# Kernel optimization log

Hardware: AMD Instinct MI355X
Metric: run time of the kernel (lower is better)

The kernel has to match this reference:

```python
import jax, jax.numpy as jnp
import numpy as np

INPUT_SIZE = 512
HIDDEN_SIZE = 1024
BATCH = 64
SEQ_LEN = 512


def _xavier(key, shape):
    fan_out, fan_in = shape
    limit = float(np.sqrt(6.0 / (fan_in + fan_out)))
    return jax.random.uniform(key, shape, jnp.float32, -limit, limit)


def setup_inputs() -> dict:
    key = jax.random.key(0)
    k = jax.random.split(key, 5)
    x = jax.random.normal(k[0], (BATCH, SEQ_LEN, INPUT_SIZE), jnp.float32)
    h0 = jnp.zeros((2, BATCH, HIDDEN_SIZE), jnp.float32)
    # layer 0: input_size -> hidden_size; layer 1: hidden_size -> hidden_size
    Wxh0 = _xavier(k[1], (HIDDEN_SIZE, INPUT_SIZE))
    Whh0 = _xavier(k[2], (HIDDEN_SIZE, HIDDEN_SIZE))
    b0 = jnp.zeros((HIDDEN_SIZE,), jnp.float32)
    Wxh1 = _xavier(k[3], (HIDDEN_SIZE, HIDDEN_SIZE))
    Whh1 = _xavier(k[4], (HIDDEN_SIZE, HIDDEN_SIZE))
    b1 = jnp.zeros((HIDDEN_SIZE,), jnp.float32)
    return {"x": x, "h0": h0, "Wxh0": Wxh0, "Whh0": Whh0, "b0": b0,
            "Wxh1": Wxh1, "Whh1": Whh1, "b1": b1}


def _rnn_layer(x_seq, h_init, Wxh, Whh, b):
    # Precompute the input projection for all timesteps (one big GEMM).
    # x_seq: [B, T, I] -> xproj: [B, T, H]
    xproj = jnp.einsum('bti,hi->bth', x_seq, Wxh) + b
    xproj_t = jnp.swapaxes(xproj, 0, 1)  # [T, B, H] for scan

    def step(h_prev, xp_t):
        h_t = jnp.tanh(xp_t + h_prev @ Whh.T)
        return h_t, h_t

    h_last, outs = jax.lax.scan(step, h_init, xproj_t)
    return jnp.swapaxes(outs, 0, 1), h_last  # [B, T, H], [B, H]


def reference(x, h0, Wxh0, Whh0, b0, Wxh1, Whh1, b1):
    out0, hn0 = _rnn_layer(x, h0[0], Wxh0, Whh0, b0)
    out1, hn1 = _rnn_layer(out0, h0[1], Wxh1, Whh1, b1)
    h_n = jnp.stack([hn0, hn1], axis=0)  # [num_layers, B, H]
    return out1, h_n
```

## Files before the change

### kernel.cpp

```cpp
#include <hip/hip_runtime.h>
#include <hip/hip_fp16.h>

typedef _Float16 f16;
typedef unsigned int u32;
typedef unsigned short u16;
typedef unsigned long long u64;
typedef _Float16 f16x8 __attribute__((ext_vector_type(8)));
typedef float f32x4 __attribute__((ext_vector_type(4)));

#define B_ 64
#define T_ 512
#define I_ 512
#define H_ 1024
#define HB_ (B_ * H_)
#define NWG_ 192
#define RS_ 32768
#define XS_ 65536

__device__ __forceinline__ u64 lda64(const u32* p) {
    return __hip_atomic_load((const u64*)p, __ATOMIC_RELAXED, __HIP_MEMORY_SCOPE_AGENT);
}
__device__ __forceinline__ u32 lda32(const u32* p) {
    return __hip_atomic_load(p, __ATOMIC_RELAXED, __HIP_MEMORY_SCOPE_AGENT);
}
__device__ __forceinline__ void sta32(u32* p, u32 v) {
    __hip_atomic_store(p, v, __ATOMIC_RELAXED, __HIP_MEMORY_SCOPE_AGENT);
}
__device__ __forceinline__ void sta16(u16* p, u16 v) {
    __hip_atomic_store(p, v, __ATOMIC_RELAXED, __HIP_MEMORY_SCOPE_AGENT);
}
__device__ __forceinline__ void stflag(int* p, int v) {
    __hip_atomic_store(p, v, __ATOMIC_RELAXED, __HIP_MEMORY_SCOPE_AGENT);
}

__device__ __forceinline__ void fastpoll(const int* p, int thr) {
    int f0, f1, f2, f3; int g = 0;
    asm volatile(
        "global_load_dword %[a], %[q], off sc0 sc1\n\t"
        "global_load_dword %[b], %[q], off sc0 sc1\n\t"
        "global_load_dword %[c], %[q], off sc0 sc1\n\t"
        "global_load_dword %[d], %[q], off sc0 sc1\n\t"
        "1:\n\t"
        "s_add_u32 %[g], %[g], 1\n\t"
        "s_cmp_gt_u32 %[g], 0x400000\n\t"
        "s_cbranch_scc1 2f\n\t"
        "s_waitcnt vmcnt(3)\n\t"
        "v_cmp_lt_i32 vcc, %[a], %[t]\n\t"
        "global_load_dword %[a], %[q], off sc0 sc1\n\t"
        "s_cbranch_vccz 2f\n\t"
        "s_waitcnt vmcnt(3)\n\t"
        "v_cmp_lt_i32 vcc, %[b], %[t]\n\t"
        "global_load_dword %[b], %[q], off sc0 sc1\n\t"
        "s_cbranch_vccz 2f\n\t"
        "s_waitcnt vmcnt(3)\n\t"
        "v_cmp_lt_i32 vcc, %[c], %[t]\n\t"
        "global_load_dword %[c], %[q], off sc0 sc1\n\t"
        "s_cbranch_vccz 2f\n\t"
        "s_waitcnt vmcnt(3)\n\t"
        "v_cmp_lt_i32 vcc, %[d], %[t]\n\t"
        "global_load_dword %[d], %[q], off sc0 sc1\n\t"
        "s_cbranch_vccnz 1b\n\t"
        "2:\n\t"
        "s_waitcnt vmcnt(0)\n\t"
        : [a]"=&v"(f0), [b]"=&v"(f1), [c]"=&v"(f2), [d]"=&v"(f3), [g]"+s"(g)
        : [q]"v"(p), [t]"v"(thr)
        : "vcc", "memory");
}

__global__ void cvt_f16(const float* __restrict__ s, f16* __restrict__ d, long n) {
    long i = ((long)blockIdx.x * blockDim.x + threadIdx.x) * 4;
    long stride = (long)gridDim.x * blockDim.x * 4;
    for (; i < n; i += stride) {
        float4 v = *reinterpret_cast<const float4*>(s + i);
        d[i+0] = (f16)v.x; d[i+1] = (f16)v.y; d[i+2] = (f16)v.z; d[i+3] = (f16)v.w;
    }
}

__global__ void init_rings(const float* __restrict__ h0,
                           u16* __restrict__ ring0, u16* __restrict__ ring1) {
    int i = blockIdx.x * blockDim.x + threadIdx.x;
    int b = i >> 10, n = i & 1023;
    int mi = b >> 4, rl = b & 15;
    int kwin = n >> 8, krem = n & 255;
    int it = krem >> 5, k32 = krem & 31;
    int kq3 = k32 >> 3, k8 = k32 & 7;
    int idx = (((mi*4 + kwin)*8 + it)*256 + (k8>>2)*128 + kq3*32 + rl*2 + ((k8>>1)&1))*2 + (k8&1);
    ring0[3*RS_*2 + idx] = __builtin_bit_cast(u16, (f16)h0[i]);
    ring1[3*RS_*2 + idx] = __builtin_bit_cast(u16, (f16)h0[HB_ + i]);
}

__global__ __launch_bounds__(256) void gemm_xproj(
    const float* __restrict__ A, const f16* __restrict__ W,
    const float* __restrict__ bias, f16* __restrict__ out)
{
    const int wave = threadIdx.x >> 6, lane = threadIdx.x & 63;
    const int m0 = blockIdx.x << 4;
    const int r = lane & 15, kq = lane >> 4;
    const int ngrp = (blockIdx.y << 9) + (wave << 7);
    const float* pa = A + (long)(m0 + r) * I_ + kq * 8;
    const f16*   pw = W + (long)(ngrp + r) * I_ + kq * 8;

    f32x4 acc[8] = {};
    #pragma unroll
    for (int kc = 0; kc < I_; kc += 32) {
        float4 a0 = *reinterpret_cast<const float4*>(pa + kc);
        float4 a1 = *reinterpret_cast<const float4*>(pa + kc + 4);
        f16x8 af = { (f16)a0.x, (f16)a0.y, (f16)a0.z, (f16)a0.w,
                     (f16)a1.x, (f16)a1.y, (f16)a1.z, (f16)a1.w };
        #pragma unroll
        for (int t = 0; t < 8; ++t) {
            f16x8 wf = *reinterpret_cast<const f16x8*>(pw + (long)t * 16 * I_ + kc);
            acc[t] = __builtin_amdgcn_mfma_f32_16x16x32_f16(af, wf, acc[t], 0, 0, 0);
        }
    }
    const int col = lane & 15, rq = lane >> 4;
    #pragma unroll
    for (int t = 0; t < 8; ++t) {
        const int n = ngrp + t * 16 + col;
        const float bv = bias[n];
        #pragma unroll
        for (int j = 0; j < 4; ++j)
            out[(long)(m0 + rq * 4 + j) * H_ + n] = (f16)(acc[t][j] + bv);
    }
}

__global__ void __launch_bounds__(256, 1) rnn_scan(
    const f16* __restrict__ Whh0, const f16* __restrict__ Wxh1, const f16* __restrict__ Whh1,
    const f16* __restrict__ xp0, const float* __restrict__ b1,
    u32* __restrict__ ring0, u32* __restrict__ ring1, u32* __restrict__ xp1,
    float* __restrict__ out, int* __restrict__ flags)
{
    extern __shared__ char smem[];
    float* part = (float*)(smem + 131072);

    const int tid = threadIdx.x;
    const int wave = tid >> 6, lane = tid & 63;
    const int wg = blockIdx.x;
    const int grp = wg >> 6, sub = wg & 63;
    const int mi = sub & 3, ct = sub >> 2;
    const int m0 = mi << 4;
    const int nbase = ct << 6;
    const int r = lane & 15, kq = lane >> 4;

    int* fAw = flags;
    int* fEw = flags + 8192;
    int* fCw = flags + 16384;
    int* fB  = flags + 24576;
    int* fD  = flags + 26624;
    const int mb4 = mi * 16;

    const f16* Wmat = (grp == 0) ? Whh0 : (grp == 1) ? Wxh1 : Whh1;

    for (int i = 0; i < 32; ++i) {
        int idx = tid + (i << 8);
        int row = idx >> 7, c = idx & 127;
        f32x4 v = *reinterpret_cast<const f32x4*>(Wmat + (long)(nbase + row) * H_ + (c << 3));
        *reinterpret_cast<f32x4*>(smem + row * 2048 + ((c ^ (row & 7)) << 4)) = v;
    }
    __syncthreads();

    const int nf = nbase + (wave << 4) + r;
    const float b1v = (grp == 1) ? b1[nf] : 0.f;

    const int kwin_s = nf >> 8, krem_s = nf & 255;
    const int it_s = krem_s >> 5, k32_s = krem_s & 31;
    const int kq3_s = k32_s >> 3, k8_s = k32_s & 7;
    const int base16 = (((mi*4 + kwin_s)*8 + it_s)*256 + (k8_s>>2)*128 + kq3_s*32 + ((k8_s>>1)&1))*2 + (k8_s&1);

    const int cBase = (mi * 4 + wave) * 2048 + (lane << 1);

    const int idx16 = lane & 15;
    const int ctp = (wave << 2) + (idx16 >> 2);
    const int wvp = idx16 & 3;
    const int myflag = ((mb4 + ct) * 4 + wave) * 32;
    const int* poll_p; int poll_d;
    if (grp == 0) {
        if (lane < 16)      { poll_p = fAw + ((mb4 + ctp) * 4 + wvp) * 32; poll_d = 0; }
        else if (lane < 32) { poll_p = fB + (mb4 + idx16) * 32;            poll_d = -3; }
        else                { poll_p = fAw + myflag;                        poll_d = -1000000; }
    } else if (grp == 1) {
        if (lane < 16)      { poll_p = fAw + ((mb4 + ctp) * 4 + wvp) * 32; poll_d = 1; }
        else if (lane == 16){ poll_p = fD + (mb4 + ct) * 32;               poll_d = -3; }
        else                { poll_p = fCw + myflag;                        poll_d = -1000000; }
    } else {
        if (lane < 16)      { poll_p = fEw + ((mb4 + ctp) * 4 + wvp) * 32; poll_d = 0; }
        else if (lane == 16){ poll_p = fCw + ((mb4 + ct) * 4 + wave) * 32; poll_d = 1; }
        else                { poll_p = fEw + myflag;                        poll_d = -1000000; }
    }

    for (int ts = 0; ts < T_; ++ts) {
        float xv[4];
        if (grp == 0) {
            #pragma unroll
            for (int j = 0; j < 4; ++j)
                xv[j] = (float)xp0[((long)(m0 + kq * 4 + j) * T_ + ts) * H_ + nf];
        } else {
            #pragma unroll
            for (int j = 0; j < 4; ++j) xv[j] = 0.f;
        }

        fastpoll(poll_p, ts + poll_d);
        __builtin_amdgcn_sched_barrier(0);

        const u32* ringA;
        if (grp == 0)      ringA = ring0 + ((ts - 1) & 3) * RS_;
        else if (grp == 1) ringA = ring0 + (ts & 3) * RS_;
        else               ringA = ring1 + ((ts - 1) & 3) * RS_;

        if (grp == 2) {
            #pragma unroll
            for (int j = 0; j < 4; ++j)
                xv[j] = __builtin_bit_cast(float,
                    lda32(xp1 + (ts & 3) * XS_ + (m0 + kq * 4 + j) * 1024 + nf));
        }

        const u32* abase = ringA + cBase;
        u64 q[8][2];
        #pragma unroll
        for (int it = 0; it < 8; ++it) {
            q[it][0] = lda64(abase + it * 256);
            q[it][1] = lda64(abase + it * 256 + 128);
        }

        f16x8 ah[8];
        #pragma unroll
        for (int it = 0; it < 8; ++it) {
            u32 w0 = (u32)q[it][0], w1 = (u32)(q[it][0] >> 32);
            u32 w2 = (u32)q[it][1], w3 = (u32)(q[it][1] >> 32);
            ah[it][0] = __builtin_bit_cast(f16, (u16)(w0 & 0xffff));
            ah[it][1] = __builtin_bit_cast(f16, (u16)(w0 >> 16));
            ah[it][2] = __builtin_bit_cast(f16, (u16)(w1 & 0xffff));
            ah[it][3] = __builtin_bit_cast(f16, (u16)(w1 >> 16));
            ah[it][4] = __builtin_bit_cast(f16, (u16)(w2 & 0xffff));
            ah[it][5] = __builtin_bit_cast(f16, (u16)(w2 >> 16));
            ah[it][6] = __builtin_bit_cast(f16, (u16)(w3 & 0xffff));
            ah[it][7] = __builtin_bit_cast(f16, (u16)(w3 >> 16));
        }
        asm volatile("s_waitcnt vmcnt(0)" ::: "memory");
        __builtin_amdgcn_sched_barrier(0);

        f32x4 acc[4] = {};
        #pragma unroll
        for (int it = 0; it < 8; ++it) {
            #pragma unroll
            for (int t = 0; t < 4; ++t) {
                f16x8 wf = *reinterpret_cast<const f16x8*>(
                    smem + (t * 16 + r) * 2048
                         + ((((wave << 5) + (it << 2) + kq) ^ (r & 7)) << 4));
                acc[t] = __builtin_amdgcn_mfma_f32_16x16x32_f16(ah[it], wf, acc[t], 0, 0, 0);
            }
        }
        #pragma unroll
        for (int t = 0; t < 4; ++t)
            *reinterpret_cast<f32x4*>(&part[((wave << 2) + t) * 256 + (lane << 2)]) = acc[t];
        __syncthreads();

        if (tid == 0) {
            if (grp == 1)      stflag(fB + (mb4 + ct) * 32, ts + 1);
            else if (grp == 2) stflag(fD + (mb4 + ct) * 32, ts + 1);
        }

        {
            f32x4 sm = *reinterpret_cast<f32x4*>(&part[wave * 256 + (lane << 2)]);
            #pragma unroll
            for (int w2 = 1; w2 < 4; ++w2)
                sm = sm + *reinterpret_cast<f32x4*>(&part[((w2 << 2) + wave) * 256 + (lane << 2)]);
            #pragma unroll
            for (int j = 0; j < 4; ++j) {
                const int b = m0 + kq * 4 + j;
                float v = sm[j];
                if (grp == 0) {
                    v = tanhf(v + xv[j]);
                    sta16((u16*)ring0 + (ts & 3) * RS_ * 2 + base16 + (kq * 4 + j) * 4,
                          __builtin_bit_cast(u16, (f16)v));
                    if (ts == T_ - 1) out[(long)B_ * T_ * H_ + (long)b * H_ + nf] = v;
                } else if (grp == 1) {
                    sta32(xp1 + (ts & 3) * XS_ + b * 1024 + nf, __builtin_bit_cast(u32, v + b1v));
                } else {
                    v = tanhf(v + xv[j]);
                    sta16((u16*)ring1 + (ts & 3) * RS_ * 2 + base16 + (kq * 4 + j) * 4,
                          __builtin_bit_cast(u16, (f16)v));
                    out[((long)b * T_ + ts) * H_ + nf] = v;
                    if (ts == T_ - 1) out[(long)B_ * T_ * H_ + HB_ + (long)b * H_ + nf] = v;
                }
            }
        }
        asm volatile("s_waitcnt vmcnt(0)" ::: "memory");
        if (lane == 0) {
            if (grp == 0)      stflag(fAw + myflag, ts + 1);
            else if (grp == 1) stflag(fCw + myflag, ts + 1);
            else               stflag(fEw + myflag, ts + 1);
        }
        __syncthreads();
    }
}

extern "C" void kernel_launch(void* const* d_in, const int* in_sizes, int n_in,
                              void* d_out, int out_size, void* d_ws, size_t ws_size,
                              hipStream_t stream) {
    const float* x    = (const float*)d_in[0];
    const float* h0   = (const float*)d_in[1];
    const float* Wxh0 = (const float*)d_in[2];
    const float* Whh0 = (const float*)d_in[3];
    const float* b0   = (const float*)d_in[4];
    const float* Wxh1 = (const float*)d_in[5];
    const float* Whh1 = (const float*)d_in[6];
    const float* b1   = (const float*)d_in[7];
    float* out = (float*)d_out;

    char* ws = (char*)d_ws;
    const long MB = 1024 * 1024;
    f16* Whh0h = (f16*)(ws + 0);
    f16* Wxh1h = (f16*)(ws + 2*MB);
    f16* Whh1h = (f16*)(ws + 4*MB);
    f16* Wxh0h = (f16*)(ws + 6*MB);
    int* flags = (int*)(ws + 7*MB);
    u32* ring0 = (u32*)(ws + 8*MB);
    u32* ring1 = (u32*)(ws + 9*MB);
    u32* xp1   = (u32*)(ws + 10*MB);
    f16* xp0   = (f16*)(ws + 16*MB);

    cvt_f16<<<512, 256, 0, stream>>>(Whh0, Whh0h, (long)H_*H_);
    cvt_f16<<<512, 256, 0, stream>>>(Wxh1, Wxh1h, (long)H_*H_);
    cvt_f16<<<512, 256, 0, stream>>>(Whh1, Whh1h, (long)H_*H_);
    cvt_f16<<<512, 256, 0, stream>>>(Wxh0, Wxh0h, (long)H_*I_);
    init_rings<<<HB_/256, 256, 0, stream>>>(h0, (u16*)ring0, (u16*)ring1);
    hipMemsetAsync(flags, 0, 128*1024, stream);

    gemm_xproj<<<dim3((B_*T_)/16, H_/512), 256, 0, stream>>>(x, Wxh0h, b0, xp0);

    hipFuncSetAttribute((const void*)rnn_scan,
                        hipFuncAttributeMaxDynamicSharedMemorySize, 147456);

    void* args[] = { (void*)&Whh0h, (void*)&Wxh1h, (void*)&Whh1h, (void*)&xp0,
                     (void*)&b1, (void*)&ring0, (void*)&ring1, (void*)&xp1,
                     (void*)&out, (void*)&flags };
    hipLaunchCooperativeKernel((void*)rnn_scan, dim3(NWG_), dim3(256), args,
                               147456, stream);
}
```

Before: 2.294 ms.

## Replace per-step flag polling with sentinel-tagged ring data and coarse progress flags

Removes the per-wave flag handshake between producer and consumer workgroups. Consumers now spin on the ring data itself until no 0xFFFF sentinel remains, and producers poison a slot a few steps ahead. The ring grows to 32 slots, and a coarse back-pressure flag is checked every 8 steps. The separate Whh/Wxh1 fp16 conversion kernels are dropped by converting fp32 weights into LDS inside the scan kernel. Risks: a real fp16 value with bit pattern 0xFFFF (a NaN) would be misread as unwritten, bounded spin loops may silently continue on timeout, and extra sentinel stores add memory traffic.

```diff
diff --git a/kernel.cpp b/kernel.cpp
--- a/kernel.cpp
+++ b/kernel.cpp
@@ -16,6 +16,8 @@
 #define NWG_ 192
 #define RS_ 32768
 #define XS_ 65536
+#define NS_ 31
+#define RL_ 8
 
 __device__ __forceinline__ u64 lda64(const u32* p) {
     return __hip_atomic_load((const u64*)p, __ATOMIC_RELAXED, __HIP_MEMORY_SCOPE_AGENT);
@@ -32,39 +34,16 @@
 __device__ __forceinline__ void stflag(int* p, int v) {
     __hip_atomic_store(p, v, __ATOMIC_RELAXED, __HIP_MEMORY_SCOPE_AGENT);
 }
-
-__device__ __forceinline__ void fastpoll(const int* p, int thr) {
-    int f0, f1, f2, f3; int g = 0;
-    asm volatile(
-        "global_load_dword %[a], %[q], off sc0 sc1\n\t"
-        "global_load_dword %[b], %[q], off sc0 sc1\n\t"
-        "global_load_dword %[c], %[q], off sc0 sc1\n\t"
-        "global_load_dword %[d], %[q], off sc0 sc1\n\t"
-        "1:\n\t"
-        "s_add_u32 %[g], %[g], 1\n\t"
-        "s_cmp_gt_u32 %[g], 0x400000\n\t"
-        "s_cbranch_scc1 2f\n\t"
-        "s_waitcnt vmcnt(3)\n\t"
-        "v_cmp_lt_i32 vcc, %[a], %[t]\n\t"
-        "global_load_dword %[a], %[q], off sc0 sc1\n\t"
-        "s_cbranch_vccz 2f\n\t"
-        "s_waitcnt vmcnt(3)\n\t"
-        "v_cmp_lt_i32 vcc, %[b], %[t]\n\t"
-        "global_load_dword %[b], %[q], off sc0 sc1\n\t"
-        "s_cbranch_vccz 2f\n\t"
-        "s_waitcnt vmcnt(3)\n\t"
-        "v_cmp_lt_i32 vcc, %[c], %[t]\n\t"
-        "global_load_dword %[c], %[q], off sc0 sc1\n\t"
-        "s_cbranch_vccz 2f\n\t"
-        "s_waitcnt vmcnt(3)\n\t"
-        "v_cmp_lt_i32 vcc, %[d], %[t]\n\t"
-        "global_load_dword %[d], %[q], off sc0 sc1\n\t"
-        "s_cbranch_vccnz 1b\n\t"
-        "2:\n\t"
-        "s_waitcnt vmcnt(0)\n\t"
-        : [a]"=&v"(f0), [b]"=&v"(f1), [c]"=&v"(f2), [d]"=&v"(f3), [g]"+s"(g)
-        : [q]"v"(p), [t]"v"(thr)
-        : "vcc", "memory");
+__device__ __forceinline__ int ldflag(const int* p) {
+    return __hip_atomic_load(p, __ATOMIC_RELAXED, __HIP_MEMORY_SCOPE_AGENT);
+}
+__device__ __forceinline__ u32 badq(u64 v) {
+    u32 lo = (u32)v, hi = (u32)(v >> 32);
+    u32 b = ((lo & 0xFFFFu) == 0xFFFFu) ? 1u : 0u;
+    b |= ((lo >> 16) == 0xFFFFu) ? 1u : 0u;
+    b |= ((hi & 0xFFFFu) == 0xFFFFu) ? 1u : 0u;
+    b |= ((hi >> 16) == 0xFFFFu) ? 1u : 0u;
+    return b;
 }
 
 __global__ void cvt_f16(const float* __restrict__ s, f16* __restrict__ d, long n) {
@@ -85,8 +64,8 @@
     int it = krem >> 5, k32 = krem & 31;
     int kq3 = k32 >> 3, k8 = k32 & 7;
     int idx = (((mi*4 + kwin)*8 + it)*256 + (k8>>2)*128 + kq3*32 + rl*2 + ((k8>>1)&1))*2 + (k8&1);
-    ring0[3*RS_*2 + idx] = __builtin_bit_cast(u16, (f16)h0[i]);
-    ring1[3*RS_*2 + idx] = __builtin_bit_cast(u16, (f16)h0[HB_ + i]);
+    ring0[NS_*RS_*2 + idx] = __builtin_bit_cast(u16, (f16)h0[i]);
+    ring1[NS_*RS_*2 + idx] = __builtin_bit_cast(u16, (f16)h0[HB_ + i]);
 }
 
 __global__ __launch_bounds__(256) void gemm_xproj(
@@ -125,7 +104,7 @@
 }
 
 __global__ void __launch_bounds__(256, 1) rnn_scan(
-    const f16* __restrict__ Whh0, const f16* __restrict__ Wxh1, const f16* __restrict__ Whh1,
+    const float* __restrict__ Whh0, const float* __restrict__ Wxh1, const float* __restrict__ Whh1,
     const f16* __restrict__ xp0, const float* __restrict__ b1,
     u32* __restrict__ ring0, u32* __restrict__ ring1, u32* __restrict__ xp1,
     float* __restrict__ out, int* __restrict__ flags)
@@ -142,20 +121,21 @@
     const int nbase = ct << 6;
     const int r = lane & 15, kq = lane >> 4;
 
-    int* fAw = flags;
-    int* fEw = flags + 8192;
-    int* fCw = flags + 16384;
-    int* fB  = flags + 24576;
-    int* fD  = flags + 26624;
+    int* prog1 = flags;
+    int* prog2 = flags + 2048;
     const int mb4 = mi * 16;
 
-    const f16* Wmat = (grp == 0) ? Whh0 : (grp == 1) ? Wxh1 : Whh1;
+    const float* Wmat = (grp == 0) ? Whh0 : (grp == 1) ? Wxh1 : Whh1;
 
     for (int i = 0; i < 32; ++i) {
         int idx = tid + (i << 8);
         int row = idx >> 7, c = idx & 127;
-        f32x4 v = *reinterpret_cast<const f32x4*>(Wmat + (long)(nbase + row) * H_ + (c << 3));
-        *reinterpret_cast<f32x4*>(smem + row * 2048 + ((c ^ (row & 7)) << 4)) = v;
+        const float* src = Wmat + (long)(nbase + row) * H_ + (c << 3);
+        float4 w0 = *reinterpret_cast<const float4*>(src);
+        float4 w1 = *reinterpret_cast<const float4*>(src + 4);
+        f16x8 wf = { (f16)w0.x, (f16)w0.y, (f16)w0.z, (f16)w0.w,
+                     (f16)w1.x, (f16)w1.y, (f16)w1.z, (f16)w1.w };
+        *reinterpret_cast<f16x8*>(smem + row * 2048 + ((c ^ (row & 7)) << 4)) = wf;
     }
     __syncthreads();
 
@@ -169,26 +149,14 @@
 
     const int cBase = (mi * 4 + wave) * 2048 + (lane << 1);
 
-    const int idx16 = lane & 15;
-    const int ctp = (wave << 2) + (idx16 >> 2);
-    const int wvp = idx16 & 3;
-    const int myflag = ((mb4 + ct) * 4 + wave) * 32;
-    const int* poll_p; int poll_d;
-    if (grp == 0) {
-        if (lane < 16)      { poll_p = fAw + ((mb4 + ctp) * 4 + wvp) * 32; poll_d = 0; }
-        else if (lane < 32) { poll_p = fB + (mb4 + idx16) * 32;            poll_d = -3; }
-        else                { poll_p = fAw + myflag;                        poll_d = -1000000; }
-    } else if (grp == 1) {
-        if (lane < 16)      { poll_p = fAw + ((mb4 + ctp) * 4 + wvp) * 32; poll_d = 1; }
-        else if (lane == 16){ poll_p = fD + (mb4 + ct) * 32;               poll_d = -3; }
-        else                { poll_p = fCw + myflag;                        poll_d = -1000000; }
-    } else {
-        if (lane < 16)      { poll_p = fEw + ((mb4 + ctp) * 4 + wvp) * 32; poll_d = 0; }
-        else if (lane == 16){ poll_p = fCw + ((mb4 + ct) * 4 + wave) * 32; poll_d = 1; }
-        else                { poll_p = fEw + myflag;                        poll_d = -1000000; }
-    }
-
     for (int ts = 0; ts < T_; ++ts) {
+        if ((ts & 7) == 0 && grp != 2 && lane < 16) {
+            const int* pf = ((grp == 0) ? prog1 : prog2) + (mb4 + lane) * 32;
+            const int thr = ts - 16;
+            int g = 0;
+            while (ldflag(pf) < thr && ++g < (1 << 20)) {}
+        }
+
         float xv[4];
         if (grp == 0) {
             #pragma unroll
@@ -199,27 +167,45 @@
             for (int j = 0; j < 4; ++j) xv[j] = 0.f;
         }
 
-        fastpoll(poll_p, ts + poll_d);
-        __builtin_amdgcn_sched_barrier(0);
-
-        const u32* ringA;
-        if (grp == 0)      ringA = ring0 + ((ts - 1) & 3) * RS_;
-        else if (grp == 1) ringA = ring0 + (ts & 3) * RS_;
-        else               ringA = ring1 + ((ts - 1) & 3) * RS_;
-
+        const u32* abase;
+        if (grp == 0)      abase = ring0 + ((ts - 1) & NS_) * RS_ + cBase;
+        else if (grp == 1) abase = ring0 + (ts & NS_) * RS_ + cBase;
+        else               abase = ring1 + ((ts - 1) & NS_) * RS_ + cBase;
+
+        u64 q[8][2];
         if (grp == 2) {
-            #pragma unroll
-            for (int j = 0; j < 4; ++j)
-                xv[j] = __builtin_bit_cast(float,
-                    lda32(xp1 + (ts & 3) * XS_ + (m0 + kq * 4 + j) * 1024 + nf));
-        }
-
-        const u32* abase = ringA + cBase;
-        u64 q[8][2];
-        #pragma unroll
-        for (int it = 0; it < 8; ++it) {
-            q[it][0] = lda64(abase + it * 256);
-            q[it][1] = lda64(abase + it * 256 + 128);
+            u32 xw[4];
+            const u32* xpb = xp1 + (ts & NS_) * XS_;
+            int g = 0; u32 bad;
+            do {
+                #pragma unroll
+                for (int it = 0; it < 8; ++it) {
+                    q[it][0] = lda64(abase + it * 256);
+                    q[it][1] = lda64(abase + it * 256 + 128);
+                }
+                #pragma unroll
+                for (int j = 0; j < 4; ++j)
+                    xw[j] = lda32(xpb + (m0 + kq * 4 + j) * 1024 + nf);
+                bad = 0;
+                #pragma unroll
+                for (int it = 0; it < 8; ++it) { bad |= badq(q[it][0]); bad |= badq(q[it][1]); }
+                #pragma unroll
+                for (int j = 0; j < 4; ++j) bad |= (xw[j] == 0xFFFFFFFFu) ? 1u : 0u;
+            } while (__any(bad != 0) && ++g < (1 << 16));
+            #pragma unroll
+            for (int j = 0; j < 4; ++j) xv[j] = __builtin_bit_cast(float, xw[j]);
+        } else {
+            int g = 0; u32 bad;
+            do {
+                #pragma unroll
+                for (int it = 0; it < 8; ++it) {
+                    q[it][0] = lda64(abase + it * 256);
+                    q[it][1] = lda64(abase + it * 256 + 128);
+                }
+                bad = 0;
+                #pragma unroll
+                for (int it = 0; it < 8; ++it) { bad |= badq(q[it][0]); bad |= badq(q[it][1]); }
+            } while (__any(bad != 0) && ++g < (1 << 16));
         }
 
         f16x8 ah[8];
@@ -236,8 +222,6 @@
             ah[it][6] = __builtin_bit_cast(f16, (u16)(w3 & 0xffff));
             ah[it][7] = __builtin_bit_cast(f16, (u16)(w3 >> 16));
         }
-        asm volatile("s_waitcnt vmcnt(0)" ::: "memory");
-        __builtin_amdgcn_sched_barrier(0);
 
         f32x4 acc[4] = {};
         #pragma unroll
@@ -255,9 +239,9 @@
             *reinterpret_cast<f32x4*>(&part[((wave << 2) + t) * 256 + (lane << 2)]) = acc[t];
         __syncthreads();
 
-        if (tid == 0) {
-            if (grp == 1)      stflag(fB + (mb4 + ct) * 32, ts + 1);
-            else if (grp == 2) stflag(fD + (mb4 + ct) * 32, ts + 1);
+        if ((ts & 7) == 7 && tid == 0) {
+            if (grp == 1)      stflag(prog1 + (mb4 + ct) * 32, ts + 1);
+            else if (grp == 2) stflag(prog2 + (mb4 + ct) * 32, ts + 1);
         }
 
         {
@@ -265,31 +249,32 @@
             #pragma unroll
             for (int w2 = 1; w2 < 4; ++w2)
                 sm = sm + *reinterpret_cast<f32x4*>(&part[((w2 << 2) + wave) * 256 + (lane << 2)]);
+            const int dSlot = (ts & NS_), rSlot = ((ts + RL_) & NS_);
             #pragma unroll
             for (int j = 0; j < 4; ++j) {
                 const int b = m0 + kq * 4 + j;
                 float v = sm[j];
                 if (grp == 0) {
                     v = tanhf(v + xv[j]);
-                    sta16((u16*)ring0 + (ts & 3) * RS_ * 2 + base16 + (kq * 4 + j) * 4,
+                    u16* p0 = (u16*)ring0;
+                    sta16(p0 + dSlot * RS_ * 2 + base16 + (kq * 4 + j) * 4,
                           __builtin_bit_cast(u16, (f16)v));
+                    sta16(p0 + rSlot * RS_ * 2 + base16 + (kq * 4 + j) * 4, (u16)0xFFFFu);
                     if (ts == T_ - 1) out[(long)B_ * T_ * H_ + (long)b * H_ + nf] = v;
                 } else if (grp == 1) {
-                    sta32(xp1 + (ts & 3) * XS_ + b * 1024 + nf, __builtin_bit_cast(u32, v + b1v));
+                    sta32(xp1 + dSlot * XS_ + b * 1024 + nf,
+                          __builtin_bit_cast(u32, v + b1v));
+                    sta32(xp1 + rSlot * XS_ + b * 1024 + nf, 0xFFFFFFFFu);
                 } else {
                     v = tanhf(v + xv[j]);
-                    sta16((u16*)ring1 + (ts & 3) * RS_ * 2 + base16 + (kq * 4 + j) * 4,
+                    u16* p1 = (u16*)ring1;
+                    sta16(p1 + dSlot * RS_ * 2 + base16 + (kq * 4 + j) * 4,
                           __builtin_bit_cast(u16, (f16)v));
+                    sta16(p1 + rSlot * RS_ * 2 + base16 + (kq * 4 + j) * 4, (u16)0xFFFFu);
                     out[((long)b * T_ + ts) * H_ + nf] = v;
                     if (ts == T_ - 1) out[(long)B_ * T_ * H_ + HB_ + (long)b * H_ + nf] = v;
                 }
             }
-        }
-        asm volatile("s_waitcnt vmcnt(0)" ::: "memory");
-        if (lane == 0) {
-            if (grp == 0)      stflag(fAw + myflag, ts + 1);
-            else if (grp == 1) stflag(fCw + myflag, ts + 1);
-            else               stflag(fEw + myflag, ts + 1);
         }
         __syncthreads();
     }
@@ -310,29 +295,24 @@
 
     char* ws = (char*)d_ws;
     const long MB = 1024 * 1024;
-    f16* Whh0h = (f16*)(ws + 0);
-    f16* Wxh1h = (f16*)(ws + 2*MB);
-    f16* Whh1h = (f16*)(ws + 4*MB);
-    f16* Wxh0h = (f16*)(ws + 6*MB);
-    int* flags = (int*)(ws + 7*MB);
-    u32* ring0 = (u32*)(ws + 8*MB);
-    u32* ring1 = (u32*)(ws + 9*MB);
-    u32* xp1   = (u32*)(ws + 10*MB);
-    f16* xp0   = (f16*)(ws + 16*MB);
-
-    cvt_f16<<<512, 256, 0, stream>>>(Whh0, Whh0h, (long)H_*H_);
-    cvt_f16<<<512, 256, 0, stream>>>(Wxh1, Wxh1h, (long)H_*H_);
-    cvt_f16<<<512, 256, 0, stream>>>(Whh1, Whh1h, (long)H_*H_);
+    f16* Wxh0h = (f16*)(ws + 0);
+    int* flags = (int*)(ws + 2*MB);
+    u32* ring0 = (u32*)(ws + 4*MB);
+    u32* ring1 = (u32*)(ws + 8*MB);
+    u32* xp1   = (u32*)(ws + 12*MB);
+    f16* xp0   = (f16*)(ws + 20*MB);
+
+    hipMemsetAsync(flags, 0, 64*1024, stream);
+    hipMemsetAsync(ws + 4*MB, 0xFF, 16*MB, stream);
     cvt_f16<<<512, 256, 0, stream>>>(Wxh0, Wxh0h, (long)H_*I_);
     init_rings<<<HB_/256, 256, 0, stream>>>(h0, (u16*)ring0, (u16*)ring1);
-    hipMemsetAsync(flags, 0, 128*1024, stream);
 
     gemm_xproj<<<dim3((B_*T_)/16, H_/512), 256, 0, stream>>>(x, Wxh0h, b0, xp0);
 
     hipFuncSetAttribute((const void*)rnn_scan,
                         hipFuncAttributeMaxDynamicSharedMemorySize, 147456);
 
-    void* args[] = { (void*)&Whh0h, (void*)&Wxh1h, (void*)&Whh1h, (void*)&xp0,
+    void* args[] = { (void*)&Whh0, (void*)&Wxh1, (void*)&Whh1, (void*)&xp0,
                      (void*)&b1, (void*)&ring0, (void*)&ring1, (void*)&xp1,
                      (void*)&out, (void*)&flags };
     hipLaunchCooperativeKernel((void*)rnn_scan, dim3(NWG_), dim3(256), args,
```

Result: faster. 2.219 ms (-3.3%).
